# Kernel tuning notes

Measured on AMD Instinct MI355X. Metric: run time of the kernel, lower is better.

The kernel has to match this reference:

```python
import jax, jax.numpy as jnp
import numpy as np

# ---- static config (matches init_kwargs) ----
B, S, E = 1, 2048, 2048
H, G, D = 32, 8, 64            # query heads, kv groups, head_dim
GS = H // G                    # group size = 4
SW = 128                       # sliding window
LAYER_IDX = 0                  # even -> sliding-window mask active
ROPE_BASE = 10000.0
ORIG_CTX = 4096.0              # yarn_original_context_length
YARN_SCALE = 2.0               # yarn_scaling_factor
BETA_FAST, BETA_SLOW = 32.0, 1.0


def _rope_sincos(position_ids):
    # YaRN-adjusted RoPE angles, computed directly at position_ids.
    freqs = 1.0 / ROPE_BASE ** (jnp.arange(0, D, 2, dtype=jnp.float32) / D)  # [D/2]
    wave_len = 2.0 * jnp.pi / freqs
    low = ORIG_CTX / BETA_FAST
    high = ORIG_CTX / BETA_SLOW
    t = jnp.clip((wave_len - low) / (high - low), 0.0, 1.0)
    eff = freqs * (1.0 - t) + (freqs / YARN_SCALE) * t
    conc = 0.1 * jnp.log(jnp.float32(YARN_SCALE)) + 1.0
    ang = position_ids[..., None].astype(jnp.float32) * eff * conc           # [B,S,D/2]
    ang = jnp.concatenate([ang, ang], axis=-1)                               # [B,S,D]
    # add head axis for broadcast over [B,H,S,D]
    return jnp.sin(ang)[:, None], jnp.cos(ang)[:, None]


def _apply_rope(x, sin, cos):
    x1, x2 = x[..., : D // 2], x[..., D // 2 :]
    rotated = jnp.concatenate([-x2, x1], axis=-1)
    return x * cos + rotated * sin


def setup_inputs() -> dict:
    key = jax.random.key(0)
    ks = jax.random.split(key, 6)
    x = jax.random.normal(ks[0], (B, S, E), dtype=jnp.float32)
    position_ids = jnp.broadcast_to(jnp.arange(S, dtype=jnp.int32), (B, S))
    # additive causal mask: -inf above the diagonal
    i = jnp.arange(S)[:, None]
    j = jnp.arange(S)[None, :]
    attn_mask = jnp.where(j > i, -jnp.inf, 0.0).astype(jnp.float32)[None, None]  # [1,1,S,S]
    sc = 0.02
    Wqkv = jax.random.normal(ks[1], ((H + 2 * G) * D, E), dtype=jnp.float32) * sc
    bqkv = jax.random.normal(ks[2], ((H + 2 * G) * D,), dtype=jnp.float32) * sc
    Wout = jax.random.normal(ks[3], (E, H * D), dtype=jnp.float32) * sc
    bout = jax.random.normal(ks[4], (E,), dtype=jnp.float32) * sc
    sinks = jax.random.normal(ks[5], (1, H, 1, 1), dtype=jnp.float32)
    return {"x": x, "position_ids": position_ids, "attn_mask": attn_mask,
            "Wqkv": Wqkv, "bqkv": bqkv, "Wout": Wout, "bout": bout, "sinks": sinks}


def reference(x, position_ids, attn_mask, Wqkv, bqkv, Wout, bout, sinks):
    b, s, _ = x.shape
    qkv = (x @ Wqkv.T + bqkv).reshape(b, s, H + 2 * G, D)
    Q = qkv[:, :, :H].transpose(0, 2, 1, 3)              # [B,H,S,D]
    K = qkv[:, :, H : H + G].transpose(0, 2, 1, 3)       # [B,G,S,D]
    V = qkv[:, :, H + G :].transpose(0, 2, 1, 3)         # [B,G,S,D]

    sin, cos = _rope_sincos(position_ids)
    Q = _apply_rope(Q, sin, cos)
    K = _apply_rope(K, sin, cos)

    # GQA: group query heads, no K/V duplication
    Qg = Q.reshape(b, G, GS, s, D)
    scores = jnp.einsum("bgmqd,bgkd->bgmqk", Qg, K) / (D ** 0.5)  # [B,G,GS,S,S]
    scores = scores.reshape(b, H, s, s) + attn_mask

    # sliding-window mask (layer_idx even, kv_len > sliding_window)
    if LAYER_IDX % 2 == 0 and s > SW:
        i = jnp.arange(s)[:, None]
        j = jnp.arange(s)[None, :]
        scores = jnp.where(j <= i - SW, -jnp.inf, scores)

    # learned sink logit prepended before softmax, then dropped
    sink = jnp.broadcast_to(sinks, (b, H, s, 1))
    attn = jax.nn.softmax(jnp.concatenate([sink, scores], axis=-1), axis=-1)[..., 1:]

    ctx = jnp.einsum("bgmqk,bgkd->bgmqd", attn.reshape(b, G, GS, s, s), V)
    ctx = ctx.reshape(b, H, s, D).transpose(0, 2, 1, 3).reshape(b, s, H * D)
    return ctx @ Wout.T + bout
```

## Files before the change

### kernel.cpp

```cpp
#include <hip/hip_runtime.h>
#include <cstdint>

#define S_LEN 2048
#define EMB   2048
#define NHEAD 32
#define NKV   8
#define HDIM  64
#define NQKV  3072

typedef __attribute__((ext_vector_type(8))) short bf16x8;
typedef __attribute__((ext_vector_type(4))) float f32x4;

#define GPTR const __attribute__((address_space(1))) void*
#define LPTR __attribute__((address_space(3))) void*

__device__ __forceinline__ unsigned short f2bf(float f){
  union { float f; unsigned int u; } v; v.f = f;
  unsigned int r = v.u + 0x7FFFu + ((v.u >> 16) & 1u);
  return (unsigned short)(r >> 16);
}
__device__ __forceinline__ float bf2f(unsigned short u){
  union { unsigned int u; float f; } v; v.u = ((unsigned int)u) << 16;
  return v.f;
}
__device__ __forceinline__ float yarn_eff(float ifr){
  const float freq = __expf(-ifr * (9.210340371976184f / 32.0f));
  const float wl = 6.283185307179586f / freq;
  float t = fminf(fmaxf((wl - 128.0f) * (1.0f / 3968.0f), 0.f), 1.f);
  return freq * (1.0f - 0.5f * t) * 1.0693147180559945f;
}

__global__ __launch_bounds__(256) void cvt3_kernel(const float* __restrict__ a, unsigned short* __restrict__ da, int na,
                                                   const float* __restrict__ b, unsigned short* __restrict__ db, int nb,
                                                   const float* __restrict__ c, unsigned short* __restrict__ dc, int nc){
  int i = blockIdx.x * 256 + threadIdx.x;
  const float* s; unsigned short* d;
  if (i < na){ s = a; d = da; }
  else if (i < na + nb){ s = b; d = db; i -= na; }
  else if (i < na + nb + nc){ s = c; d = dc; i -= na + nb; }
  else return;
  const float4 v = ((const float4*)s)[i];
  ushort4 o;
  o.x = f2bf(v.x); o.y = f2bf(v.y); o.z = f2bf(v.z); o.w = f2bf(v.w);
  ((ushort4*)d)[i] = o;
}

template<int OUT_BF16, int ROPE, int TM>
__global__ __launch_bounds__(256) void gemm_bt(const unsigned short* __restrict__ A,
                                               const unsigned short* __restrict__ B,
                                               const float* __restrict__ bias,
                                               void* __restrict__ Cout,
                                               const int* __restrict__ pos,
                                               int M, int N, int K){
  constexpr int MI = TM / 32;
  constexpr int AI = TM / 64;
  constexpr int VI = 2 * (AI + 2);
  __shared__ unsigned short As[4*TM*32];
  __shared__ unsigned short Bs[4*128*32];
  const int tid  = threadIdx.x;
  const int lane = tid & 63;
  const int wid  = tid >> 6;
  const int m0 = blockIdx.y * TM;
  const int n0 = blockIdx.x * 128;
  const int wm = (wid >> 1) * (TM/2);
  const int wn = (wid & 1) * 64;
  const int fm = lane & 15;
  const int q8 = (lane >> 4) * 8;
  const int quad = lane >> 4;

  f32x4 acc[MI][4];
#pragma unroll
  for (int i = 0; i < MI; ++i)
#pragma unroll
    for (int j = 0; j < 4; ++j) acc[i][j] = {0.f, 0.f, 0.f, 0.f};

  const int srow = lane >> 2;
  const int scol = (lane & 3) * 8;
  const unsigned short* Ag = A + (size_t)(m0 + wid*(TM/4) + srow) * K + scol;
  const unsigned short* Bg = B + (size_t)(n0 + wid*32 + srow) * K + scol;
  unsigned short* AsW = &As[(wid*(TM/4))*32];
  unsigned short* BsW = &Bs[(wid*32)*32];

  auto stage_sub = [&](int k0, int slot){
    unsigned short* dA = AsW + slot*(TM*32);
    unsigned short* dB = BsW + slot*(128*32);
#pragma unroll
    for (int t = 0; t < AI; ++t)
      __builtin_amdgcn_global_load_lds((GPTR)(Ag + k0 + (size_t)(t*16)*K), (LPTR)(dA + t*16*32), 16, 0, 0);
    __builtin_amdgcn_global_load_lds((GPTR)(Bg + k0), (LPTR)dB, 16, 0, 0);
    __builtin_amdgcn_global_load_lds((GPTR)(Bg + k0 + (size_t)16*K), (LPTR)(dB + 16*32), 16, 0, 0);
  };

  stage_sub(0, 0);  stage_sub(32, 1);
  stage_sub(64, 2); stage_sub(96, 3);

  const int KEP = K >> 6;
  for (int e = 0; e < KEP; ++e){
    const int buf = e & 1;
    if (e + 1 < KEP){
      if constexpr (TM == 128) asm volatile("s_waitcnt vmcnt(8)" ::: "memory");
      else                     asm volatile("s_waitcnt vmcnt(6)" ::: "memory");
    } else {
      asm volatile("s_waitcnt vmcnt(0)" ::: "memory");
    }
    asm volatile("s_barrier" ::: "memory");

    bf16x8 af[2][MI], bfr[2][4];
#pragma unroll
    for (int s = 0; s < 2; ++s){
      const unsigned short* Ab = As + (buf*2+s)*(TM*32);
      const unsigned short* Bb = Bs + (buf*2+s)*(128*32);
#pragma unroll
      for (int i = 0; i < MI; ++i) af[s][i]  = *(const bf16x8*)&Ab[(wm + i*16 + fm)*32 + q8];
#pragma unroll
      for (int j = 0; j < 4; ++j)  bfr[s][j] = *(const bf16x8*)&Bb[(wn + j*16 + fm)*32 + q8];
    }
#pragma unroll
    for (int s = 0; s < 2; ++s)
#pragma unroll
      for (int i = 0; i < MI; ++i)
#pragma unroll
        for (int j = 0; j < 4; ++j)
          acc[i][j] = __builtin_amdgcn_mfma_f32_16x16x32_bf16(af[s][i], bfr[s][j], acc[i][j], 0, 0, 0);

    asm volatile("s_barrier" ::: "memory");
    if (e + 2 < KEP){
      stage_sub((e+2)*64,      buf*2);
      stage_sub((e+2)*64 + 32, buf*2 + 1);
    }
  }

  float bv[4];
#pragma unroll
  for (int j = 0; j < 4; ++j) bv[j] = bias[n0 + wn + j*16 + fm];

  const bool dorope = ROPE && (n0 + wn) < 2560;
  if (dorope){
    const float eff0 = yarn_eff((float)fm);
    const float eff1 = yarn_eff((float)(fm + 16));
#pragma unroll
    for (int i = 0; i < MI; ++i){
#pragma unroll
      for (int r = 0; r < 4; ++r){
        const int row = m0 + wm + i*16 + quad*4 + r;
        const float pp = (float)pos[row];
        float s0, c0, s1, c1;
        __sincosf(pp * eff0, &s0, &c0);
        __sincosf(pp * eff1, &s1, &c1);
        const float v0 = acc[i][0][r] + bv[0];
        const float v1 = acc[i][1][r] + bv[1];
        const float v2 = acc[i][2][r] + bv[2];
        const float v3 = acc[i][3][r] + bv[3];
        const float o0 = v0*c0 - v2*s0;
        const float o1 = v1*c1 - v3*s1;
        const float o2 = v2*c0 + v0*s0;
        const float o3 = v3*c1 + v1*s1;
        const size_t base = (size_t)row*N + n0 + wn + fm;
        if (OUT_BF16){
          unsigned short* C16 = (unsigned short*)Cout;
          C16[base +  0] = f2bf(o0); C16[base + 16] = f2bf(o1);
          C16[base + 32] = f2bf(o2); C16[base + 48] = f2bf(o3);
        } else {
          float* C32 = (float*)Cout;
          C32[base +  0] = o0; C32[base + 16] = o1;
          C32[base + 32] = o2; C32[base + 48] = o3;
        }
      }
    }
  } else {
#pragma unroll
    for (int i = 0; i < MI; ++i){
#pragma unroll
      for (int r = 0; r < 4; ++r){
        const int row = m0 + wm + i*16 + quad*4 + r;
        const size_t base = (size_t)row*N + n0 + wn + fm;
#pragma unroll
        for (int j = 0; j < 4; ++j){
          const float v = acc[i][j][r] + bv[j];
          if (OUT_BF16) ((unsigned short*)Cout)[base + j*16] = f2bf(v);
          else          ((float*)Cout)[base + j*16] = v;
        }
      }
    }
  }
}

__global__ __launch_bounds__(256) void attn_kernel(const unsigned short* __restrict__ qkv,
                                                   const float* __restrict__ sinks,
                                                   unsigned short* __restrict__ ctxb){
  const int h  = blockIdx.y;
  const int q0 = blockIdx.x * 64;
  const int g  = h >> 2;
  const int tid  = threadIdx.x;
  const int lane = tid & 63;
  const int wid  = tid >> 6;
  const int fm   = lane & 15;
  const int quad = lane >> 4;

  __shared__ unsigned short Ks[2*64*40];
  __shared__ unsigned short Vt[2*64*34];
  __shared__ unsigned short Pl[4*2*16*40];

  const int qrow = q0 + wid*16 + fm;
  bf16x8 aq[2];
#pragma unroll
  for (int ks = 0; ks < 2; ++ks)
    aq[ks] = *(const bf16x8*)(qkv + (size_t)qrow*NQKV + h*HDIM + ks*32 + quad*8);

  f32x4 o[4];
#pragma unroll
  for (int nt = 0; nt < 4; ++nt) o[nt] = {0.f, 0.f, 0.f, 0.f};
  float m_[4], l_[4];
#pragma unroll
  for (int r = 0; r < 4; ++r){ m_[r] = -30000.f; l_[r] = 0.f; }

  const int qbase = q0 + wid*16 + quad*4;
  int cs0 = q0 - 128; if (cs0 < 0) cs0 = 0;
  unsigned short* plw = &Pl[wid*1280];

  for (int cs = cs0; cs <= q0; cs += 64){
    __syncthreads();
#pragma unroll
    for (int it = 0; it < 2; ++it){
      const int e = (tid + it*256) * 8;
      const int key = e >> 6, d0 = e & 63;
      const unsigned short* kp = qkv + (size_t)(cs + key)*NQKV + EMB + g*HDIM + d0;
      *(bf16x8*)&Ks[(d0>>5)*2560 + key*40 + (d0 & 31)] = *(const bf16x8*)kp;
      const bf16x8 vv = *(const bf16x8*)(kp + NKV*HDIM);
      const unsigned short* vs = (const unsigned short*)&vv;
      unsigned short* vt = &Vt[(key>>5)*2176 + (key & 31)];
#pragma unroll
      for (int j = 0; j < 8; ++j) vt[(d0 + j)*34] = vs[j];
    }
    __syncthreads();

    f32x4 sa[4];
#pragma unroll
    for (int nt = 0; nt < 4; ++nt){
      sa[nt] = {0.f, 0.f, 0.f, 0.f};
#pragma unroll
      for (int ks = 0; ks < 2; ++ks){
        const bf16x8 bk = *(const bf16x8*)&Ks[ks*2560 + (nt*16 + fm)*40 + quad*8];
        sa[nt] = __builtin_amdgcn_mfma_f32_16x16x32_bf16(aq[ks], bk, sa[nt], 0, 0, 0);
      }
    }

#pragma unroll
    for (int nt = 0; nt < 4; ++nt){
      const int key = cs + nt*16 + fm;
#pragma unroll
      for (int r = 0; r < 4; ++r){
        const float s = sa[nt][r] * 0.125f;
        const bool ok = (unsigned)(qbase + r - key) < 128u;
        sa[nt][r] = ok ? s : -1e30f;
      }
    }

#pragma unroll
    for (int r = 0; r < 4; ++r){
      float t = fmaxf(fmaxf(sa[0][r], sa[1][r]), fmaxf(sa[2][r], sa[3][r]));
#pragma unroll
      for (int off = 1; off < 16; off <<= 1) t = fmaxf(t, __shfl_xor(t, off, 64));
      const float nm = fmaxf(m_[r], t);
      const float al = __expf(m_[r] - nm);
#pragma unroll
      for (int nt = 0; nt < 4; ++nt) sa[nt][r] = __expf(sa[nt][r] - nm);
      float ts = (sa[0][r] + sa[1][r]) + (sa[2][r] + sa[3][r]);
#pragma unroll
      for (int off = 1; off < 16; off <<= 1) ts += __shfl_xor(ts, off, 64);
      l_[r] = l_[r]*al + ts;
      m_[r] = nm;
#pragma unroll
      for (int nt = 0; nt < 4; ++nt) o[nt][r] *= al;
    }

#pragma unroll
    for (int nt = 0; nt < 4; ++nt)
#pragma unroll
      for (int r = 0; r < 4; ++r)
        plw[(nt>>1)*640 + (quad*4 + r)*40 + (nt&1)*16 + fm] = f2bf(sa[nt][r]);
    __asm__ volatile("s_waitcnt lgkmcnt(0)" ::: "memory");

    bf16x8 pa[2];
#pragma unroll
    for (int ks = 0; ks < 2; ++ks)
      pa[ks] = *(const bf16x8*)&plw[ks*640 + fm*40 + quad*8];
    const unsigned int* vb = (const unsigned int*)Vt;
#pragma unroll
    for (int nt = 0; nt < 4; ++nt){
#pragma unroll
      for (int ks = 0; ks < 2; ++ks){
        const int ui = ks*1088 + (nt*16 + fm)*17 + quad*4;
        union { unsigned int u[4]; bf16x8 v; } bb;
        bb.u[0] = vb[ui+0]; bb.u[1] = vb[ui+1]; bb.u[2] = vb[ui+2]; bb.u[3] = vb[ui+3];
        o[nt] = __builtin_amdgcn_mfma_f32_16x16x32_bf16(pa[ks], bb.v, o[nt], 0, 0, 0);
      }
    }
  }

  const float snk = sinks[h];
#pragma unroll
  for (int r = 0; r < 4; ++r){
    const float nm = fmaxf(m_[r], snk);
    const float e  = __expf(m_[r] - nm);
    const float denom = l_[r]*e + __expf(snk - nm);
    const float sc = e / denom;
    const size_t row = (size_t)(qbase + r)*EMB + h*HDIM;
#pragma unroll
    for (int nt = 0; nt < 4; ++nt)
      ctxb[row + nt*16 + fm] = f2bf(o[nt][r] * sc);
  }
}

extern "C" void kernel_launch(void* const* d_in, const int* in_sizes, int n_in,
                              void* d_out, int out_size, void* d_ws, size_t ws_size,
                              hipStream_t stream){
  const float* x     = (const float*)d_in[0];
  const int*   pos   = (const int*)  d_in[1];
  const float* Wqkv  = (const float*)d_in[3];
  const float* bqkv  = (const float*)d_in[4];
  const float* Wout  = (const float*)d_in[5];
  const float* bout  = (const float*)d_in[6];
  const float* sinks = (const float*)d_in[7];

  char* ws = (char*)d_ws;
  unsigned short* xb   = (unsigned short*)(ws);
  unsigned short* wqb  = (unsigned short*)(ws + 8388608);
  unsigned short* wob  = (unsigned short*)(ws + 20971520);
  unsigned short* qkv  = (unsigned short*)(ws + 29360128);
  unsigned short* ctxb = (unsigned short*)(ws + 41943040);

  cvt3_kernel<<<dim3(14336), dim3(256), 0, stream>>>(x, xb, 1048576,
                                                     Wqkv, wqb, 1572864,
                                                     Wout, wob, 1048576);

  gemm_bt<1,1,128><<<dim3(24, 16), dim3(256), 0, stream>>>(xb, wqb, bqkv, (void*)qkv, pos, 2048, 3072, 2048);
  attn_kernel<<<dim3(32, 32), dim3(256), 0, stream>>>(qkv, sinks, ctxb);
  gemm_bt<0,0,64><<<dim3(16, 32), dim3(256), 0, stream>>>(ctxb, wob, bout, d_out, nullptr, 2048, 2048, 2048);
}
```

Baseline: 199.4 us.

## Add XOR-swizzled LDS, 12-wave QKV GEMM tile, and fuse Wout cast into attention

Applies an XOR swizzle to the LDS column layout in both GEMMs to reduce bank conflicts on fragment reads. Adds a dedicated QKV GEMM kernel with 768-thread blocks and 128x192 tiles, launching 256 blocks (one per CU) instead of 384, with RoPE fused into its epilogue. Moves the Wout fp32-to-bf16 conversion out of the cast kernel and into the tail of the attention kernel so it runs alongside attention work. The larger block raises register pressure, and the tail conversion lengthens each attention block.

```diff
diff --git a/kernel.cpp b/kernel.cpp
--- a/kernel.cpp
+++ b/kernel.cpp
@@ -45,6 +45,7 @@
   ((ushort4*)d)[i] = o;
 }
 
+
 template<int OUT_BF16, int ROPE, int TM>
 __global__ __launch_bounds__(256) void gemm_bt(const unsigned short* __restrict__ A,
                                                const unsigned short* __restrict__ B,
@@ -54,7 +55,6 @@
                                                int M, int N, int K){
   constexpr int MI = TM / 32;
   constexpr int AI = TM / 64;
-  constexpr int VI = 2 * (AI + 2);
   __shared__ unsigned short As[4*TM*32];
   __shared__ unsigned short Bs[4*128*32];
   const int tid  = threadIdx.x;
@@ -65,8 +65,8 @@
   const int wm = (wid >> 1) * (TM/2);
   const int wn = (wid & 1) * 64;
   const int fm = lane & 15;
-  const int q8 = (lane >> 4) * 8;
   const int quad = lane >> 4;
+  const int csw8 = (quad ^ ((fm >> 1) & 3)) * 8;
 
   f32x4 acc[MI][4];
 #pragma unroll
@@ -75,7 +75,7 @@
     for (int j = 0; j < 4; ++j) acc[i][j] = {0.f, 0.f, 0.f, 0.f};
 
   const int srow = lane >> 2;
-  const int scol = (lane & 3) * 8;
+  const int scol = (((lane & 3) ^ ((lane >> 3) & 3)) * 8);
   const unsigned short* Ag = A + (size_t)(m0 + wid*(TM/4) + srow) * K + scol;
   const unsigned short* Bg = B + (size_t)(n0 + wid*32 + srow) * K + scol;
   unsigned short* AsW = &As[(wid*(TM/4))*32];
@@ -111,9 +111,9 @@
       const unsigned short* Ab = As + (buf*2+s)*(TM*32);
       const unsigned short* Bb = Bs + (buf*2+s)*(128*32);
 #pragma unroll
-      for (int i = 0; i < MI; ++i) af[s][i]  = *(const bf16x8*)&Ab[(wm + i*16 + fm)*32 + q8];
-#pragma unroll
-      for (int j = 0; j < 4; ++j)  bfr[s][j] = *(const bf16x8*)&Bb[(wn + j*16 + fm)*32 + q8];
+      for (int i = 0; i < MI; ++i) af[s][i]  = *(const bf16x8*)&Ab[(wm + i*16 + fm)*32 + csw8];
+#pragma unroll
+      for (int j = 0; j < 4; ++j)  bfr[s][j] = *(const bf16x8*)&Bb[(wn + j*16 + fm)*32 + csw8];
     }
 #pragma unroll
     for (int s = 0; s < 2; ++s)
@@ -185,9 +185,132 @@
   }
 }
 
+__global__ __launch_bounds__(768) void gemm_qkv(const unsigned short* __restrict__ A,
+                                                const unsigned short* __restrict__ B,
+                                                const float* __restrict__ bias,
+                                                unsigned short* __restrict__ C,
+                                                const int* __restrict__ pos){
+  constexpr int M = 2048, N = 3072, K = 2048;
+  __shared__ unsigned short As[4*128*32];
+  __shared__ unsigned short Bs[4*192*32];
+  const int tid  = threadIdx.x;
+  const int lane = tid & 63;
+  const int wid  = tid >> 6;
+  const int m0 = blockIdx.y * 128;
+  const int n0 = blockIdx.x * 192;
+  const int wm = (wid & 3) * 32;
+  const int wn = (wid >> 2) * 64;
+  const int fm = lane & 15;
+  const int quad = lane >> 4;
+  const int csw8 = (quad ^ ((fm >> 1) & 3)) * 8;
+
+  f32x4 acc[2][4];
+#pragma unroll
+  for (int i = 0; i < 2; ++i)
+#pragma unroll
+    for (int j = 0; j < 4; ++j) acc[i][j] = {0.f, 0.f, 0.f, 0.f};
+
+  const int srow = lane >> 2;
+  const int scol = (((lane & 3) ^ ((lane >> 3) & 3)) * 8);
+
+  auto stage = [&](int k0, int slot2){
+    for (int u = wid; u < 40; u += 12){
+      const int sub = (u >= 20) ? 1 : 0;
+      const int idx = u - sub*20;
+      const int kk  = k0 + sub*32;
+      if (idx < 8){
+        const unsigned short* src = A + (size_t)(m0 + idx*16 + srow) * K + scol + kk;
+        __builtin_amdgcn_global_load_lds((GPTR)src, (LPTR)(&As[0] + (slot2+sub)*(128*32) + idx*16*32), 16, 0, 0);
+      } else {
+        const int r = (idx - 8) * 16;
+        const unsigned short* src = B + (size_t)(n0 + r + srow) * K + scol + kk;
+        __builtin_amdgcn_global_load_lds((GPTR)src, (LPTR)(&Bs[0] + (slot2+sub)*(192*32) + r*32), 16, 0, 0);
+      }
+    }
+  };
+
+  stage(0, 0);
+  stage(64, 2);
+
+  constexpr int KEP = K >> 6;
+  for (int e = 0; e < KEP; ++e){
+    const int buf = e & 1;
+    if (e + 1 < KEP) asm volatile("s_waitcnt vmcnt(3)" ::: "memory");
+    else             asm volatile("s_waitcnt vmcnt(0)" ::: "memory");
+    asm volatile("s_barrier" ::: "memory");
+
+    bf16x8 af[2][2], bfr[2][4];
+#pragma unroll
+    for (int s = 0; s < 2; ++s){
+      const unsigned short* Ab = As + (buf*2+s)*(128*32);
+      const unsigned short* Bb = Bs + (buf*2+s)*(192*32);
+#pragma unroll
+      for (int i = 0; i < 2; ++i) af[s][i]  = *(const bf16x8*)&Ab[(wm + i*16 + fm)*32 + csw8];
+#pragma unroll
+      for (int j = 0; j < 4; ++j) bfr[s][j] = *(const bf16x8*)&Bb[(wn + j*16 + fm)*32 + csw8];
+    }
+#pragma unroll
+    for (int s = 0; s < 2; ++s)
+#pragma unroll
+      for (int i = 0; i < 2; ++i)
+#pragma unroll
+        for (int j = 0; j < 4; ++j)
+          acc[i][j] = __builtin_amdgcn_mfma_f32_16x16x32_bf16(af[s][i], bfr[s][j], acc[i][j], 0, 0, 0);
+
+    asm volatile("s_barrier" ::: "memory");
+    if (e + 2 < KEP) stage((e+2)*64, buf*2);
+  }
+
+  float bv[4];
+#pragma unroll
+  for (int j = 0; j < 4; ++j) bv[j] = bias[n0 + wn + j*16 + fm];
+
+  const bool dorope = (n0 + wn) < 2560;
+  if (dorope){
+    const float eff0 = yarn_eff((float)fm);
+    const float eff1 = yarn_eff((float)(fm + 16));
+#pragma unroll
+    for (int i = 0; i < 2; ++i){
+#pragma unroll
+      for (int r = 0; r < 4; ++r){
+        const int row = m0 + wm + i*16 + quad*4 + r;
+        const float pp = (float)pos[row];
+        float s0, c0, s1, c1;
+        __sincosf(pp * eff0, &s0, &c0);
+        __sincosf(pp * eff1, &s1, &c1);
+        const float v0 = acc[i][0][r] + bv[0];
+        const float v1 = acc[i][1][r] + bv[1];
+        const float v2 = acc[i][2][r] + bv[2];
+        const float v3 = acc[i][3][r] + bv[3];
+        const float o0 = v0*c0 - v2*s0;
+        const float o1 = v1*c1 - v3*s1;
+        const float o2 = v2*c0 + v0*s0;
+        const float o3 = v3*c1 + v1*s1;
+        const size_t base = (size_t)row*N + n0 + wn + fm;
+        C[base +  0] = f2bf(o0); C[base + 16] = f2bf(o1);
+        C[base + 32] = f2bf(o2); C[base + 48] = f2bf(o3);
+      }
+    }
+  } else {
+#pragma unroll
+    for (int i = 0; i < 2; ++i){
+#pragma unroll
+      for (int r = 0; r < 4; ++r){
+        const int row = m0 + wm + i*16 + quad*4 + r;
+        const size_t base = (size_t)row*N + n0 + wn + fm;
+#pragma unroll
+        for (int j = 0; j < 4; ++j)
+          C[base + j*16] = f2bf(acc[i][j][r] + bv[j]);
+      }
+    }
+  }
+}
+
 __global__ __launch_bounds__(256) void attn_kernel(const unsigned short* __restrict__ qkv,
                                                    const float* __restrict__ sinks,
-                                                   unsigned short* __restrict__ ctxb){
+                                                   unsigned short* __restrict__ ctxb,
+                                                   const float* __restrict__ wout,
+                                                   unsigned short* __restrict__ wob){
   const int h  = blockIdx.y;
   const int q0 = blockIdx.x * 64;
   const int g  = h >> 2;
@@ -309,6 +432,16 @@
 #pragma unroll
     for (int nt = 0; nt < 4; ++nt)
       ctxb[row + nt*16 + fm] = f2bf(o[nt][r] * sc);
+  }
+
+  const int gtid = (blockIdx.y * 32 + blockIdx.x) * 256 + tid;
+#pragma unroll
+  for (int it = 0; it < 4; ++it){
+    const int i4 = gtid + it * (32*32*256);
+    const float4 v = ((const float4*)wout)[i4];
+    ushort4 ow;
+    ow.x = f2bf(v.x); ow.y = f2bf(v.y); ow.z = f2bf(v.z); ow.w = f2bf(v.w);
+    ((ushort4*)wob)[i4] = ow;
   }
 }
 
@@ -330,11 +463,11 @@
   unsigned short* qkv  = (unsigned short*)(ws + 29360128);
   unsigned short* ctxb = (unsigned short*)(ws + 41943040);
 
-  cvt3_kernel<<<dim3(14336), dim3(256), 0, stream>>>(x, xb, 1048576,
+  cvt3_kernel<<<dim3(10240), dim3(256), 0, stream>>>(x, xb, 1048576,
                                                      Wqkv, wqb, 1572864,
-                                                     Wout, wob, 1048576);
-
-  gemm_bt<1,1,128><<<dim3(24, 16), dim3(256), 0, stream>>>(xb, wqb, bqkv, (void*)qkv, pos, 2048, 3072, 2048);
-  attn_kernel<<<dim3(32, 32), dim3(256), 0, stream>>>(qkv, sinks, ctxb);
+                                                     nullptr, nullptr, 0);
+
+  gemm_qkv<<<dim3(16, 16), dim3(768), 0, stream>>>(xb, wqb, bqkv, qkv, pos);
+  attn_kernel<<<dim3(32, 32), dim3(256), 0, stream>>>(qkv, sinks, ctxb, Wout, wob);
   gemm_bt<0,0,64><<<dim3(16, 32), dim3(256), 0, stream>>>(ctxb, wob, bout, d_out, nullptr, 2048, 2048, 2048);
 }
```

New measurement: 203.6 us. 2.1% more time.
